# Kernel tuning notes

Measured on AMD Instinct MI355X. Metric: run time of the kernel, lower is better.

Reference implementation:

```python
import jax, jax.numpy as jnp
import numpy as np

N_EMB = 768
HEAD_SIZE = 64
B, T = 256, 256


def setup_inputs() -> dict:
    key = jax.random.key(0)
    kx, kq, kk, kv = jax.random.split(key, 4)
    x = jax.random.normal(kx, (B, T, N_EMB), dtype=jnp.float32)
    # nn.Linear(n_emb, head_size, bias=False): store as [in, out], apply x @ W
    s = 1.0 / np.sqrt(N_EMB)
    Wq = jax.random.uniform(kq, (N_EMB, HEAD_SIZE), jnp.float32, -s, s)
    Wk = jax.random.uniform(kk, (N_EMB, HEAD_SIZE), jnp.float32, -s, s)
    Wv = jax.random.uniform(kv, (N_EMB, HEAD_SIZE), jnp.float32, -s, s)
    return {"x": x, "Wq": Wq, "Wk": Wk, "Wv": Wv}


def reference(x, Wq, Wk, Wv):
    # x: [B, T, C]
    q = x @ Wq  # [B, T, H]
    k = x @ Wk  # [B, T, H]
    v = x @ Wv  # [B, T, H]
    scale = k.shape[-1] ** (-0.5)
    wei = jnp.einsum('bth,bsh->bts', q, k) * scale  # [B, T, T]
    t = x.shape[1]
    causal = jnp.tril(jnp.ones((t, t), dtype=bool))  # [T, T]
    wei = jnp.where(causal, wei, -jnp.inf)
    wei = jax.nn.softmax(wei, axis=-1)
    out = jnp.einsum('bts,bsh->bth', wei, v)  # [B, T, H]
    return out
```

## Files before the change

kernel.cpp:

```cpp
#include <hip/hip_runtime.h>
#include <hip/hip_bf16.h>
#include <stdint.h>


typedef __attribute__((ext_vector_type(8))) short short8;
typedef __attribute__((ext_vector_type(4))) short short4v;
typedef __attribute__((ext_vector_type(4))) float f32x4;

#define MFMA16(a, b, c) __builtin_amdgcn_mfma_f32_16x16x32_bf16(a, b, c, 0, 0, 0)

#define BAR() do { \
  asm volatile("s_waitcnt lgkmcnt(0)" ::: "memory"); \
  __builtin_amdgcn_s_barrier(); \
} while (0)

static __device__ __forceinline__ unsigned short f2bf(float f) {
  union { float f; uint32_t u; } v; v.f = f;
  return (unsigned short)((v.u + 0x7FFFu + ((v.u >> 16) & 1u)) >> 16);
}

__global__ void wt_prep(const float* __restrict__ Wq, const float* __restrict__ Wk,
                        const float* __restrict__ Wv, unsigned short* __restrict__ WtT) {
  int idx = blockIdx.x * 256 + threadIdx.x;
  if (idx >= 147456) return;
  int co = idx & 63;
  int c = (idx >> 6) & 31;
  int itm = idx >> 11;
  int it = itm / 3;
  int m = itm - it * 3;
  const float* W = (m == 0) ? Wq : (m == 1 ? Wk : Wv);
  float v = W[(it * 32 + c) * 64 + co];
  if (m == 0) v *= 0.125f;
  WtT[it * 7680 + (m * 64 + co) * 40 + c] = f2bf(v);
}

#define XS0 0
#define XS1 20480
#define WS0 40960
#define WS1 56320
#define KOFF 71680
#define VOFF 104448

__global__ __launch_bounds__(512, 2) void fused_head(
    const float* __restrict__ x, const unsigned short* __restrict__ WtT,
    float* __restrict__ out) {
  __shared__ char smem[137216];
  const int tid = threadIdx.x;
  const int w = tid >> 6;
  const int lane = tid & 63;
  const int l15 = lane & 15, g = lane >> 4;
  const int b = blockIdx.x;
  const float* xB = x + (size_t)b * 256 * 768;

  char* xs0 = smem + XS0;
  char* xs1 = smem + XS1;
  char* ws0 = smem + WS0;
  char* ws1 = smem + WS1;

  f32x4 acc[2][12];
  #pragma unroll
  for (int rt = 0; rt < 2; ++rt)
    #pragma unroll
    for (int ct = 0; ct < 12; ++ct) acc[rt][ct] = f32x4{0.f, 0.f, 0.f, 0.f};

  const int sxr = tid >> 3;
  const int sxc = tid & 7;
  const bool stv = (tid < 480);

  float4 xA[4], xPB[4];
  short8 wA[2], wPB[2];

  auto loadX = [&](float4* xr, int kk) {
    #pragma unroll
    for (int p = 0; p < 4; ++p)
      xr[p] = *reinterpret_cast<const float4*>(
          xB + (size_t)(p * 64 + sxr) * 768 + kk + sxc * 4);
  };
  auto loadW = [&](short8* wr, int it) {
    if (stv) {
      const short8* s = reinterpret_cast<const short8*>(WtT + (size_t)it * 7680 + tid * 16);
      wr[0] = s[0]; wr[1] = s[1];
    }
  };
  auto storeX = [&](char* xsb, const float4* xr) {
    #pragma unroll
    for (int p = 0; p < 4; ++p) {
      short4v v;
      v[0] = (short)f2bf(xr[p].x); v[1] = (short)f2bf(xr[p].y);
      v[2] = (short)f2bf(xr[p].z); v[3] = (short)f2bf(xr[p].w);
      *reinterpret_cast<short4v*>(xsb + (p * 64 + sxr) * 80 + sxc * 8) = v;
    }
  };
  auto storeW = [&](char* wsb, const short8* wr) {
    if (stv) {
      *reinterpret_cast<short8*>(wsb + tid * 32) = wr[0];
      *reinterpret_cast<short8*>(wsb + tid * 32 + 16) = wr[1];
    }
  };
  auto compute = [&](const char* xsb, const char* wsb) {
    short8 a0 = *reinterpret_cast<const short8*>(xsb + (w * 32 + l15) * 80 + g * 16);
    short8 a1 = *reinterpret_cast<const short8*>(xsb + (w * 32 + 16 + l15) * 80 + g * 16);
    #pragma unroll
    for (int ct = 0; ct < 12; ++ct) {
      short8 bb = *reinterpret_cast<const short8*>(wsb + (ct * 16 + l15) * 80 + g * 16);
      acc[0][ct] = MFMA16(a0, bb, acc[0][ct]);
      acc[1][ct] = MFMA16(a1, bb, acc[1][ct]);
    }
  };

  loadX(xA, 0); loadW(wA, 0);
  storeX(xs0, xA); storeW(ws0, wA);
  loadX(xPB, 32); loadW(wPB, 1);
  BAR();

  for (int j = 0; j < 12; ++j) {
    if (2 * j + 2 < 24) { loadX(xA, (2 * j + 2) * 32); loadW(wA, 2 * j + 2); }
    compute(xs0, ws0);
    storeX(xs1, xPB); storeW(ws1, wPB);
    BAR();
    if (2 * j + 3 < 24) { loadX(xPB, (2 * j + 3) * 32); loadW(wPB, 2 * j + 3); }
    compute(xs1, ws1);
    if (2 * j + 2 < 24) { storeX(xs0, xA); storeW(ws0, wA); }
    BAR();
  }

  char* Kl = smem + KOFF;
  char* Vl = smem + VOFF;
  char* Ql = smem;
  #pragma unroll
  for (int rt = 0; rt < 2; ++rt) {
    #pragma unroll
    for (int ct = 0; ct < 4; ++ct) {
      #pragma unroll
      for (int r = 0; r < 4; ++r) {
        int key = w * 32 + rt * 16 + g * 4 + r;
        int h = ct * 16 + l15;
        *reinterpret_cast<unsigned short*>(
            Kl + key * 128 + ((h * 2) ^ ((key & 7) << 4))) = f2bf(acc[rt][4 + ct][r]);
        *reinterpret_cast<unsigned short*>(
            Ql + key * 256 + ((h * 2) ^ ((key & 15) << 4))) = f2bf(acc[rt][ct][r]);
      }
      int h = ct * 16 + l15;
      int t0 = w * 32 + rt * 16 + g * 4;
      short4v pv;
      pv[0] = (short)f2bf(acc[rt][8 + ct][0]); pv[1] = (short)f2bf(acc[rt][8 + ct][1]);
      pv[2] = (short)f2bf(acc[rt][8 + ct][2]); pv[3] = (short)f2bf(acc[rt][8 + ct][3]);
      *reinterpret_cast<short4v*>(Vl + h * 512 + ((t0 * 2) ^ ((h & 7) << 4))) = pv;
    }
  }
  BAR();

  short8 qf[2][2];
  #pragma unroll
  for (int rt = 0; rt < 2; ++rt) {
    const int qrow0 = (rt == 0) ? w * 16 : (15 - w) * 16;
    #pragma unroll
    for (int c = 0; c < 2; ++c) {
      int row = qrow0 + l15;
      qf[rt][c] = *reinterpret_cast<const short8*>(
          Ql + row * 256 + ((c * 64 + g * 16) ^ ((row & 15) << 4)));
    }
  }
  BAR();

  char* Pw = smem + w * 8192;

  #pragma unroll
  for (int rt = 0; rt < 2; ++rt) {
    const int tile_idx = (rt == 0) ? w : 15 - w;
    const int trow0 = tile_idx * 16;
    const int ntile = tile_idx + 1;
    const int pswz = (l15 & 7) << 4;

    f32x4 s[16];
    #pragma unroll
    for (int t = 0; t < 16; ++t) {
      if (t < ntile) {
        int key = t * 16 + l15;
        int kswz = (key & 7) << 4;
        short8 k0 = *reinterpret_cast<const short8*>(Kl + key * 128 + ((g * 16) ^ kswz));
        short8 k1 = *reinterpret_cast<const short8*>(Kl + key * 128 + ((64 + g * 16) ^ kswz));
        f32x4 a = f32x4{0.f, 0.f, 0.f, 0.f};
        a = MFMA16(k0, qf[rt][0], a);
        a = MFMA16(k1, qf[rt][1], a);
        s[t] = a;
      }
    }

    float sum = 0.f;
    #pragma unroll
    for (int t = 0; t < 16; ++t) {
      if (t < ntile) {
        const bool diag = (t == ntile - 1);
        short4v pk;
        #pragma unroll
        for (int r = 0; r < 4; ++r) {
          float p = __expf(s[t][r]);
          if (diag && (g * 4 + r > l15)) p = 0.f;
          sum += p;
          pk[r] = (short)f2bf(p);
        }
        *reinterpret_cast<short4v*>(Pw + l15 * 512 + ((t * 32 + g * 8) ^ pswz)) = pk;
      }
    }
    if (ntile & 1) {
      *reinterpret_cast<short4v*>(Pw + l15 * 512 + ((ntile * 32 + g * 8) ^ pswz)) =
          short4v{0, 0, 0, 0};
    }
    sum += __shfl_xor(sum, 16);
    sum += __shfl_xor(sum, 32);
    const float inv = 1.0f / sum;

    const int nkc = (ntile + 1) >> 1;
    f32x4 o[4];
    #pragma unroll
    for (int i = 0; i < 4; ++i) o[i] = f32x4{0.f, 0.f, 0.f, 0.f};
    #pragma unroll
    for (int kc = 0; kc < 8; ++kc) {
      if (kc < nkc) {
        short8 pa = *reinterpret_cast<const short8*>(
            Pw + l15 * 512 + ((kc * 64 + g * 16) ^ pswz));
        #pragma unroll
        for (int ht = 0; ht < 4; ++ht) {
          int h = ht * 16 + l15;
          short8 bv = *reinterpret_cast<const short8*>(
              Vl + h * 512 + ((kc * 64 + g * 16) ^ ((h & 7) << 4)));
          o[ht] = MFMA16(bv, pa, o[ht]);
        }
      }
    }

    {
      float* dst = out + ((size_t)b * 256 + trow0 + l15) * 64 + g * 4;
      #pragma unroll
      for (int ht = 0; ht < 4; ++ht) {
        float4 ov;
        ov.x = o[ht][0] * inv; ov.y = o[ht][1] * inv;
        ov.z = o[ht][2] * inv; ov.w = o[ht][3] * inv;
        *reinterpret_cast<float4*>(dst + ht * 16) = ov;
      }
    }
  }
}

extern "C" void kernel_launch(void* const* d_in, const int* in_sizes, int n_in,
                              void* d_out, int out_size, void* d_ws, size_t ws_size,
                              hipStream_t stream) {
  const float* x  = (const float*)d_in[0];
  const float* Wq = (const float*)d_in[1];
  const float* Wk = (const float*)d_in[2];
  const float* Wv = (const float*)d_in[3];
  unsigned short* WtT = (unsigned short*)d_ws;
  float* out = (float*)d_out;

  hipLaunchKernelGGL(wt_prep, dim3(576), dim3(256), 0, stream, Wq, Wk, Wv, WtT);
  hipLaunchKernelGGL(fused_head, dim3(256), dim3(512), 0, stream, x, WtT, out);
}
```

Baseline: 48.10 us.

## Stream x and weight tiles straight into LDS with global_load_lds

Replaces the register-staged x/W loads (load to VGPRs, convert to bf16, store to LDS) with asynchronous global_load_lds DMA of raw fp32 x and pre-padded bf16 weights into double-buffered LDS. The bf16 conversion moves to the LDS read side, and vmcnt waits plus barriers replace the old register ping-pong. This aims to cut VGPR pressure and instruction overhead in the projection loop. The price is twice the LDS for x, since it is held as fp32, which raises the LDS size and drops launch bounds to one block per CU, losing the two-block occupancy.

Measured after the change: 48.99 us. Within noise of the previous version (+1.9%).

```diff
diff --git a/kernel.cpp b/kernel.cpp
--- a/kernel.cpp
+++ b/kernel.cpp
@@ -13,6 +13,13 @@
   asm volatile("s_waitcnt lgkmcnt(0)" ::: "memory"); \
   __builtin_amdgcn_s_barrier(); \
 } while (0)
+#define VMWAIT(N) asm volatile("s_waitcnt vmcnt(" #N ")" ::: "memory")
+
+typedef const __attribute__((address_space(1))) uint32_t glb_u32;
+typedef __attribute__((address_space(3))) uint32_t lds_u32;
+static __device__ __forceinline__ void gload16(const void* g, void* l) {
+  __builtin_amdgcn_global_load_lds((glb_u32*)g, (lds_u32*)l, 16, 0, 0);
+}
 
 static __device__ __forceinline__ unsigned short f2bf(float f) {
   union { float f; uint32_t u; } v; v.f = f;
@@ -31,31 +38,26 @@
   const float* W = (m == 0) ? Wq : (m == 1 ? Wk : Wv);
   float v = W[(it * 32 + c) * 64 + co];
   if (m == 0) v *= 0.125f;
-  WtT[it * 7680 + (m * 64 + co) * 40 + c] = f2bf(v);
-}
-
-#define XS0 0
-#define XS1 20480
-#define WS0 40960
-#define WS1 56320
-#define KOFF 71680
-#define VOFF 104448
-
-__global__ __launch_bounds__(512, 2) void fused_head(
+  WtT[it * 8192 + (m * 64 + co) * 40 + c] = f2bf(v);
+}
+
+#define XS_ 0
+#define WS_ 65536
+#define KOFF 98304
+#define VOFF 131072
+
+__global__ __launch_bounds__(512, 1) void fused_head(
     const float* __restrict__ x, const unsigned short* __restrict__ WtT,
     float* __restrict__ out) {
-  __shared__ char smem[137216];
+  __shared__ char smem[163840];
   const int tid = threadIdx.x;
   const int w = tid >> 6;
   const int lane = tid & 63;
   const int l15 = lane & 15, g = lane >> 4;
+  const int l7 = lane & 7, l8 = lane >> 3;
   const int b = blockIdx.x;
   const float* xB = x + (size_t)b * 256 * 768;
-
-  char* xs0 = smem + XS0;
-  char* xs1 = smem + XS1;
-  char* ws0 = smem + WS0;
-  char* ws1 = smem + WS1;
+  const char* WtB = (const char*)WtT;
 
   f32x4 acc[2][12];
   #pragma unroll
@@ -63,43 +65,36 @@
     #pragma unroll
     for (int ct = 0; ct < 12; ++ct) acc[rt][ct] = f32x4{0.f, 0.f, 0.f, 0.f};
 
-  const int sxr = tid >> 3;
-  const int sxc = tid & 7;
-  const bool stv = (tid < 480);
-
-  float4 xA[4], xPB[4];
-  short8 wA[2], wPB[2];
-
-  auto loadX = [&](float4* xr, int kk) {
-    #pragma unroll
-    for (int p = 0; p < 4; ++p)
-      xr[p] = *reinterpret_cast<const float4*>(
-          xB + (size_t)(p * 64 + sxr) * 768 + kk + sxc * 4);
+  const int xsw = (l7 * 16) ^ (l8 << 4);
+
+  auto issue_tile = [&](int it) {
+    const int p = it & 1;
+    char* xd = smem + XS_ + p * 32768 + w * 4096;
+    const float* xg = xB + (size_t)(w * 32 + l8) * 768 + it * 32 + (xsw >> 2);
+    #pragma unroll
+    for (int c = 0; c < 4; ++c)
+      gload16(xg + (size_t)c * 8 * 768, xd + c * 1024);
+    char* wd = smem + WS_ + p * 16384 + w * 2048;
+    const char* wg = WtB + (size_t)it * 16384 + w * 2048 + lane * 16;
+    gload16(wg, wd);
+    gload16(wg + 1024, wd + 1024);
   };
-  auto loadW = [&](short8* wr, int it) {
-    if (stv) {
-      const short8* s = reinterpret_cast<const short8*>(WtT + (size_t)it * 7680 + tid * 16);
-      wr[0] = s[0]; wr[1] = s[1];
-    }
-  };
-  auto storeX = [&](char* xsb, const float4* xr) {
-    #pragma unroll
-    for (int p = 0; p < 4; ++p) {
-      short4v v;
-      v[0] = (short)f2bf(xr[p].x); v[1] = (short)f2bf(xr[p].y);
-      v[2] = (short)f2bf(xr[p].z); v[3] = (short)f2bf(xr[p].w);
-      *reinterpret_cast<short4v*>(xsb + (p * 64 + sxr) * 80 + sxc * 8) = v;
-    }
-  };
-  auto storeW = [&](char* wsb, const short8* wr) {
-    if (stv) {
-      *reinterpret_cast<short8*>(wsb + tid * 32) = wr[0];
-      *reinterpret_cast<short8*>(wsb + tid * 32 + 16) = wr[1];
-    }
+
+  const int ar7 = (l15 & 7) << 4;
+  auto lda = [&](const char* xsb, int rt) {
+    const char* rowp = xsb + (w * 32 + rt * 16 + l15) * 128;
+    f32x4 f0 = *reinterpret_cast<const f32x4*>(rowp + ((g * 32) ^ ar7));
+    f32x4 f1 = *reinterpret_cast<const f32x4*>(rowp + ((g * 32 + 16) ^ ar7));
+    short8 a;
+    a[0] = (short)f2bf(f0[0]); a[1] = (short)f2bf(f0[1]);
+    a[2] = (short)f2bf(f0[2]); a[3] = (short)f2bf(f0[3]);
+    a[4] = (short)f2bf(f1[0]); a[5] = (short)f2bf(f1[1]);
+    a[6] = (short)f2bf(f1[2]); a[7] = (short)f2bf(f1[3]);
+    return a;
   };
   auto compute = [&](const char* xsb, const char* wsb) {
-    short8 a0 = *reinterpret_cast<const short8*>(xsb + (w * 32 + l15) * 80 + g * 16);
-    short8 a1 = *reinterpret_cast<const short8*>(xsb + (w * 32 + 16 + l15) * 80 + g * 16);
+    short8 a0 = lda(xsb, 0);
+    short8 a1 = lda(xsb, 1);
     #pragma unroll
     for (int ct = 0; ct < 12; ++ct) {
       short8 bb = *reinterpret_cast<const short8*>(wsb + (ct * 16 + l15) * 80 + g * 16);
@@ -108,20 +103,15 @@
     }
   };
 
-  loadX(xA, 0); loadW(wA, 0);
-  storeX(xs0, xA); storeW(ws0, wA);
-  loadX(xPB, 32); loadW(wPB, 1);
-  BAR();
-
-  for (int j = 0; j < 12; ++j) {
-    if (2 * j + 2 < 24) { loadX(xA, (2 * j + 2) * 32); loadW(wA, 2 * j + 2); }
-    compute(xs0, ws0);
-    storeX(xs1, xPB); storeW(ws1, wPB);
+  issue_tile(0);
+  issue_tile(1);
+  for (int n = 0; n < 24; ++n) {
+    const int p = n & 1;
+    if (n < 23) { VMWAIT(6); } else { VMWAIT(0); }
+    __builtin_amdgcn_s_barrier();
+    compute(smem + XS_ + p * 32768, smem + WS_ + p * 16384);
     BAR();
-    if (2 * j + 3 < 24) { loadX(xPB, (2 * j + 3) * 32); loadW(wPB, 2 * j + 3); }
-    compute(xs1, ws1);
-    if (2 * j + 2 < 24) { storeX(xs0, xA); storeW(ws0, wA); }
-    BAR();
+    if (n + 2 < 24) issue_tile(n + 2);
   }
 
   char* Kl = smem + KOFF;
```

## Load x directly into MFMA A-fragments, bypassing LDS staging

Applied to the files above, without the earlier changes.

Each wave now reads its own x rows from global memory straight into registers laid out as MFMA A-operands and converts them to bf16 in registers, with no LDS round trip. This removes the x LDS stores, the LDS reads and the associated bank traffic. The cost is less coalesced global loads: each lane reads 32 contiguous bytes per row instead of the whole block streaming full rows. Only the weights still go through LDS double buffering.

After: 50.95 us. 5.9% more time.

```diff
diff --git a/kernel.cpp b/kernel.cpp
--- a/kernel.cpp
+++ b/kernel.cpp
@@ -17,6 +17,15 @@
 static __device__ __forceinline__ unsigned short f2bf(float f) {
   union { float f; uint32_t u; } v; v.f = f;
   return (unsigned short)((v.u + 0x7FFFu + ((v.u >> 16) & 1u)) >> 16);
+}
+
+static __device__ __forceinline__ short8 conv8(float4 lo, float4 hi) {
+  short8 a;
+  a[0] = (short)f2bf(lo.x); a[1] = (short)f2bf(lo.y);
+  a[2] = (short)f2bf(lo.z); a[3] = (short)f2bf(lo.w);
+  a[4] = (short)f2bf(hi.x); a[5] = (short)f2bf(hi.y);
+  a[6] = (short)f2bf(hi.z); a[7] = (short)f2bf(hi.w);
+  return a;
 }
 
 __global__ void wt_prep(const float* __restrict__ Wq, const float* __restrict__ Wk,
@@ -34,8 +43,6 @@
   WtT[it * 7680 + (m * 64 + co) * 40 + c] = f2bf(v);
 }
 
-#define XS0 0
-#define XS1 20480
 #define WS0 40960
 #define WS1 56320
 #define KOFF 71680
@@ -52,8 +59,6 @@
   const int b = blockIdx.x;
   const float* xB = x + (size_t)b * 256 * 768;
 
-  char* xs0 = smem + XS0;
-  char* xs1 = smem + XS1;
   char* ws0 = smem + WS0;
   char* ws1 = smem + WS1;
 
@@ -63,18 +68,18 @@
     #pragma unroll
     for (int ct = 0; ct < 12; ++ct) acc[rt][ct] = f32x4{0.f, 0.f, 0.f, 0.f};
 
-  const int sxr = tid >> 3;
-  const int sxc = tid & 7;
   const bool stv = (tid < 480);
+  const float* xp0 = xB + (size_t)(w * 32 + l15) * 768 + g * 8;
+  const float* xp1 = xp0 + 16 * 768;
 
   float4 xA[4], xPB[4];
   short8 wA[2], wPB[2];
 
   auto loadX = [&](float4* xr, int kk) {
-    #pragma unroll
-    for (int p = 0; p < 4; ++p)
-      xr[p] = *reinterpret_cast<const float4*>(
-          xB + (size_t)(p * 64 + sxr) * 768 + kk + sxc * 4);
+    xr[0] = *reinterpret_cast<const float4*>(xp0 + kk);
+    xr[1] = *reinterpret_cast<const float4*>(xp0 + kk + 4);
+    xr[2] = *reinterpret_cast<const float4*>(xp1 + kk);
+    xr[3] = *reinterpret_cast<const float4*>(xp1 + kk + 4);
   };
   auto loadW = [&](short8* wr, int it) {
     if (stv) {
@@ -82,24 +87,13 @@
       wr[0] = s[0]; wr[1] = s[1];
     }
   };
-  auto storeX = [&](char* xsb, const float4* xr) {
-    #pragma unroll
-    for (int p = 0; p < 4; ++p) {
-      short4v v;
-      v[0] = (short)f2bf(xr[p].x); v[1] = (short)f2bf(xr[p].y);
-      v[2] = (short)f2bf(xr[p].z); v[3] = (short)f2bf(xr[p].w);
-      *reinterpret_cast<short4v*>(xsb + (p * 64 + sxr) * 80 + sxc * 8) = v;
-    }
-  };
   auto storeW = [&](char* wsb, const short8* wr) {
     if (stv) {
       *reinterpret_cast<short8*>(wsb + tid * 32) = wr[0];
       *reinterpret_cast<short8*>(wsb + tid * 32 + 16) = wr[1];
     }
   };
-  auto compute = [&](const char* xsb, const char* wsb) {
-    short8 a0 = *reinterpret_cast<const short8*>(xsb + (w * 32 + l15) * 80 + g * 16);
-    short8 a1 = *reinterpret_cast<const short8*>(xsb + (w * 32 + 16 + l15) * 80 + g * 16);
+  auto mfma12 = [&](short8 a0, short8 a1, const char* wsb) {
     #pragma unroll
     for (int ct = 0; ct < 12; ++ct) {
       short8 bb = *reinterpret_cast<const short8*>(wsb + (ct * 16 + l15) * 80 + g * 16);
@@ -108,20 +102,30 @@
     }
   };
 
-  loadX(xA, 0); loadW(wA, 0);
-  storeX(xs0, xA); storeW(ws0, wA);
-  loadX(xPB, 32); loadW(wPB, 1);
+  loadW(wA, 0);
+  storeW(ws0, wA);
+  loadX(xA, 0);
+  loadX(xPB, 32);
+  loadW(wPB, 1);
   BAR();
 
   for (int j = 0; j < 12; ++j) {
-    if (2 * j + 2 < 24) { loadX(xA, (2 * j + 2) * 32); loadW(wA, 2 * j + 2); }
-    compute(xs0, ws0);
-    storeX(xs1, xPB); storeW(ws1, wPB);
-    BAR();
-    if (2 * j + 3 < 24) { loadX(xPB, (2 * j + 3) * 32); loadW(wPB, 2 * j + 3); }
-    compute(xs1, ws1);
-    if (2 * j + 2 < 24) { storeX(xs0, xA); storeW(ws0, wA); }
-    BAR();
+    {
+      short8 a0 = conv8(xA[0], xA[1]);
+      short8 a1 = conv8(xA[2], xA[3]);
+      if (2 * j + 2 < 24) { loadX(xA, (2 * j + 2) * 32); loadW(wA, 2 * j + 2); }
+      mfma12(a0, a1, ws0);
+      storeW(ws1, wPB);
+      BAR();
+    }
+    {
+      short8 a0 = conv8(xPB[0], xPB[1]);
+      short8 a1 = conv8(xPB[2], xPB[3]);
+      if (2 * j + 3 < 24) { loadX(xPB, (2 * j + 3) * 32); loadW(wPB, 2 * j + 3); }
+      mfma12(a0, a1, ws1);
+      if (2 * j + 2 < 24) storeW(ws0, wA);
+      BAR();
+    }
   }
 
   char* Kl = smem + KOFF;
```

## Double the projection K-tile to 64 and switch LDS padding to XOR swizzle

Applied to the files above, without the earlier changes.

The QKV projection loop now stages 64 input channels per iteration instead of 32, halving the number of pipeline stages and barriers (12 instead of 24). LDS rows for x and the weight tiles drop their padding and use an XOR swizzle to avoid bank conflicts, and the weight prep kernel writes the swizzled layout directly. This raises per-thread register staging (8 float4 plus 4 short8 buffers, twice) and LDS footprint per stage, which could pressure occupancy at 512 threads with 2 blocks per CU.

Result: slower. 81.05 us (+68.5%).

```diff
diff --git a/kernel.cpp b/kernel.cpp
--- a/kernel.cpp
+++ b/kernel.cpp
@@ -24,27 +24,28 @@
   int idx = blockIdx.x * 256 + threadIdx.x;
   if (idx >= 147456) return;
   int co = idx & 63;
-  int c = (idx >> 6) & 31;
-  int itm = idx >> 11;
+  int c = (idx >> 6) & 63;
+  int itm = idx >> 12;
   int it = itm / 3;
   int m = itm - it * 3;
   const float* W = (m == 0) ? Wq : (m == 1 ? Wk : Wv);
-  float v = W[(it * 32 + c) * 64 + co];
+  float v = W[(it * 64 + c) * 64 + co];
   if (m == 0) v *= 0.125f;
-  WtT[it * 7680 + (m * 64 + co) * 40 + c] = f2bf(v);
+  int row = m * 64 + co;
+  WtT[it * 12288 + row * 64 + (c ^ ((row & 7) << 3))] = f2bf(v);
 }
 
 #define XS0 0
-#define XS1 20480
-#define WS0 40960
-#define WS1 56320
-#define KOFF 71680
-#define VOFF 104448
+#define XS1 32768
+#define WS0 65536
+#define WS1 90112
+#define KOFF 65536
+#define VOFF 98304
 
 __global__ __launch_bounds__(512, 2) void fused_head(
     const float* __restrict__ x, const unsigned short* __restrict__ WtT,
     float* __restrict__ out) {
-  __shared__ char smem[137216];
+  __shared__ char smem[131072];
   const int tid = threadIdx.x;
   const int w = tid >> 6;
   const int lane = tid & 63;
@@ -63,65 +64,86 @@
     #pragma unroll
     for (int ct = 0; ct < 12; ++ct) acc[rt][ct] = f32x4{0.f, 0.f, 0.f, 0.f};
 
-  const int sxr = tid >> 3;
-  const int sxc = tid & 7;
-  const bool stv = (tid < 480);
-
-  float4 xA[4], xPB[4];
-  short8 wA[2], wPB[2];
-
-  auto loadX = [&](float4* xr, int kk) {
-    #pragma unroll
-    for (int p = 0; p < 4; ++p)
-      xr[p] = *reinterpret_cast<const float4*>(
-          xB + (size_t)(p * 64 + sxr) * 768 + kk + sxc * 4);
+  const int sc = tid & 15;
+  const int sr0 = tid >> 4;
+  const bool stv = (tid < 384);
+
+  float4 xA[8], xPB[8];
+  short8 wA[4], wPB[4];
+
+  auto loadX = [&](float4* xr, int it) {
+    const float* src = xB + (size_t)sr0 * 768 + it * 64 + sc * 4;
+    #pragma unroll
+    for (int p = 0; p < 8; ++p)
+      xr[p] = *reinterpret_cast<const float4*>(src + (size_t)p * 32 * 768);
   };
   auto loadW = [&](short8* wr, int it) {
     if (stv) {
-      const short8* s = reinterpret_cast<const short8*>(WtT + (size_t)it * 7680 + tid * 16);
-      wr[0] = s[0]; wr[1] = s[1];
+      const char* src = (const char*)WtT + (size_t)it * 24576 + tid * 16;
+      #pragma unroll
+      for (int k = 0; k < 4; ++k)
+        wr[k] = *reinterpret_cast<const short8*>(src + k * 6144);
     }
   };
   auto storeX = [&](char* xsb, const float4* xr) {
     #pragma unroll
-    for (int p = 0; p < 4; ++p) {
+    for (int p = 0; p < 8; ++p) {
+      int row = p * 32 + sr0;
       short4v v;
       v[0] = (short)f2bf(xr[p].x); v[1] = (short)f2bf(xr[p].y);
       v[2] = (short)f2bf(xr[p].z); v[3] = (short)f2bf(xr[p].w);
-      *reinterpret_cast<short4v*>(xsb + (p * 64 + sxr) * 80 + sxc * 8) = v;
+      *reinterpret_cast<short4v*>(xsb + row * 128 + ((sc * 8) ^ ((row & 7) << 4))) = v;
     }
   };
   auto storeW = [&](char* wsb, const short8* wr) {
     if (stv) {
-      *reinterpret_cast<short8*>(wsb + tid * 32) = wr[0];
-      *reinterpret_cast<short8*>(wsb + tid * 32 + 16) = wr[1];
+      #pragma unroll
+      for (int k = 0; k < 4; ++k)
+        *reinterpret_cast<short8*>(wsb + tid * 16 + k * 6144) = wr[k];
     }
   };
   auto compute = [&](const char* xsb, const char* wsb) {
-    short8 a0 = *reinterpret_cast<const short8*>(xsb + (w * 32 + l15) * 80 + g * 16);
-    short8 a1 = *reinterpret_cast<const short8*>(xsb + (w * 32 + 16 + l15) * 80 + g * 16);
-    #pragma unroll
-    for (int ct = 0; ct < 12; ++ct) {
-      short8 bb = *reinterpret_cast<const short8*>(wsb + (ct * 16 + l15) * 80 + g * 16);
-      acc[0][ct] = MFMA16(a0, bb, acc[0][ct]);
-      acc[1][ct] = MFMA16(a1, bb, acc[1][ct]);
+    #pragma unroll
+    for (int kh = 0; kh < 2; ++kh) {
+      short8 a0, a1;
+      {
+        int r0 = w * 32 + l15;
+        int r1 = r0 + 16;
+        a0 = *reinterpret_cast<const short8*>(
+            xsb + r0 * 128 + ((kh * 64 + g * 16) ^ ((r0 & 7) << 4)));
+        a1 = *reinterpret_cast<const short8*>(
+            xsb + r1 * 128 + ((kh * 64 + g * 16) ^ ((r1 & 7) << 4)));
+      }
+      #pragma unroll
+      for (int ct = 0; ct < 12; ++ct) {
+        int row = ct * 16 + l15;
+        short8 bb = *reinterpret_cast<const short8*>(
+            wsb + row * 128 + ((kh * 64 + g * 16) ^ ((row & 7) << 4)));
+        acc[0][ct] = MFMA16(a0, bb, acc[0][ct]);
+        acc[1][ct] = MFMA16(a1, bb, acc[1][ct]);
+      }
     }
   };
 
   loadX(xA, 0); loadW(wA, 0);
   storeX(xs0, xA); storeW(ws0, wA);
-  loadX(xPB, 32); loadW(wPB, 1);
+  loadX(xPB, 1); loadW(wPB, 1);
   BAR();
 
-  for (int j = 0; j < 12; ++j) {
-    if (2 * j + 2 < 24) { loadX(xA, (2 * j + 2) * 32); loadW(wA, 2 * j + 2); }
-    compute(xs0, ws0);
-    storeX(xs1, xPB); storeW(ws1, wPB);
-    BAR();
-    if (2 * j + 3 < 24) { loadX(xPB, (2 * j + 3) * 32); loadW(wPB, 2 * j + 3); }
-    compute(xs1, ws1);
-    if (2 * j + 2 < 24) { storeX(xs0, xA); storeW(ws0, wA); }
-    BAR();
+  #pragma unroll 1
+  for (int jo = 0; jo < 6; ++jo) {
+    {
+      if (jo < 5) { loadX(xA, 2 * jo + 2); loadW(wA, 2 * jo + 2); }
+      compute(xs0, ws0);
+      storeX(xs1, xPB); storeW(ws1, wPB);
+      BAR();
+    }
+    {
+      if (jo < 5) { loadX(xPB, 2 * jo + 3); loadW(wPB, 2 * jo + 3); }
+      compute(xs1, ws1);
+      if (jo < 5) { storeX(xs0, xA); storeW(ws0, wA); }
+      BAR();
+    }
   }
 
   char* Kl = smem + KOFF;
```
